# Kernel optimization log

Measured on AMD Instinct MI355X. Metric: run time of the kernel, lower is better.

## Reference

```python
import math
import jax, jax.numpy as jnp
import numpy as np

HIDDEN = 128
NUM_REL = 48
NUM_BASES = 8
NUM_ENT = 50000
NUM_SPECIAL = 64
NUM_EDGES = 600000


def setup_inputs() -> dict:
    key = jax.random.key(0)
    ks = jax.random.split(key, 8)
    edge_index = jax.random.randint(ks[0], (2, NUM_EDGES), 0, NUM_ENT, dtype=jnp.int64)
    edge_type = jax.random.randint(ks[1], (NUM_EDGES,), 0, NUM_REL, dtype=jnp.int64)
    # node embeddings: uniform(-stdv, stdv), stdv = sqrt(6/(N+d)) as in the torch init
    stdv = math.sqrt(6.0 / (NUM_ENT + HIDDEN))
    node_embeds = jax.random.uniform(ks[2], (NUM_ENT, HIDDEN), jnp.float32, -stdv, stdv)
    # RGCN basis-decomposition params (PyG RGCNConv): weight [B, d, d], comp [R, B]
    basis = jax.random.normal(ks[3], (NUM_BASES, HIDDEN, HIDDEN), jnp.float32) * (1.0 / math.sqrt(HIDDEN))
    comp = jax.random.normal(ks[4], (NUM_REL, NUM_BASES), jnp.float32) * (1.0 / math.sqrt(NUM_BASES))
    root = jax.random.normal(ks[5], (HIDDEN, HIDDEN), jnp.float32) * (1.0 / math.sqrt(HIDDEN))
    bias = jnp.zeros((HIDDEN,), jnp.float32)
    special_emb = jax.random.normal(ks[6], (NUM_SPECIAL, HIDDEN), jnp.float32) * 0.02
    special_emb = special_emb.at[0].set(0.0)  # padding_idx=0
    return {"edge_index": edge_index, "edge_type": edge_type,
            "node_embeds": node_embeds, "basis": basis, "comp": comp,
            "root": root, "bias": bias, "special_emb": special_emb}


def rgcn_conv(x, edge_index, edge_type, basis, comp, root, bias):
    # PyG RGCNConv with basis decomposition, aggr='mean', root weight + bias.
    # W_r = sum_b comp[r, b] * basis[b]; out[n] = x[n] @ root + bias
    #        + sum_r mean_{e: type(e)=r, dst(e)=n} (x[src(e)] @ W_r)
    N = x.shape[0]
    R, B = comp.shape
    src, dst = edge_index[0], edge_index[1]
    # per-(relation, dst) in-degree for the per-relation mean aggregation
    seg = edge_type * N + dst  # [E]
    cnt = jax.ops.segment_sum(jnp.ones(src.shape[0], x.dtype), seg, num_segments=R * N)
    norm = 1.0 / jnp.maximum(cnt[seg], 1.0)  # [E]
    w = comp[edge_type] * norm[:, None]  # [E, B] per-edge basis coefficients / count
    x_src = x[src]  # [E, d] gather (dominant memory traffic)
    out = x @ root + bias  # [N, d]
    # linearity: mean over edges of (x_src @ W) == (weighted-sum of x_src) @ basis_b per basis
    for b in range(B):
        agg = jax.ops.segment_sum(x_src * w[:, b:b + 1], dst, num_segments=N)  # [N, d]
        out = out + agg @ basis[b]
    return out


def reference(edge_index, edge_type, node_embeds, basis, comp, root, bias, special_emb):
    node_out = rgcn_conv(node_embeds, edge_index, edge_type, basis, comp, root, bias)
    return jnp.concatenate([node_out, special_emb], axis=0)  # [N + S, d]
```

## Files before the change

kernel.cpp:

```cpp
#include <hip/hip_runtime.h>

#define NDIM 128
#define NBASES 8
#define KDIM 1152
#define GTILE 16
#define APITCH 1160

typedef __attribute__((ext_vector_type(8))) __bf16 bfrag;
typedef __attribute__((ext_vector_type(4))) float f32x4;

__device__ __forceinline__ float bf2f(unsigned short b) {
    return __uint_as_float(((unsigned)b) << 16);
}
__device__ __forceinline__ unsigned short f2bf(float f) {
    unsigned u = __float_as_uint(f);
    unsigned r = u + 0x7FFFu + ((u >> 16) & 1u);
    return (unsigned short)(r >> 16);
}
__device__ __forceinline__ unsigned pack2bf(float lo, float hi) {
    return (unsigned)f2bf(lo) | ((unsigned)f2bf(hi) << 16);
}
__device__ __forceinline__ float loadF(const void* p, int idx, int isf32) {
    return isf32 ? ((const float*)p)[idx] : bf2f(((const unsigned short*)p)[idx]);
}

__global__ void detect_k(const unsigned short* __restrict__ xs,
                         const int* __restrict__ ei, int* __restrict__ meta) {
    if (threadIdx.x != 0 || blockIdx.x != 0) return;
    const uint4* xv = (const uint4*)xs;
    unsigned f32m = 0;
    uint4 bx[16];
    #pragma unroll
    for (int i = 0; i < 16; ++i) bx[i] = xv[i];
    #pragma unroll
    for (int i = 0; i < 16; ++i) {
        unsigned a = bx[i].x, b = bx[i].y, c = bx[i].z, d = bx[i].w;
        f32m |= (((a & 0xFFFFu) >> 7) & 0xFFu) > 124u;
        f32m |= (((b & 0xFFFFu) >> 7) & 0xFFu) > 124u;
        f32m |= (((c & 0xFFFFu) >> 7) & 0xFFu) > 124u;
        f32m |= (((d & 0xFFFFu) >> 7) & 0xFFu) > 124u;
    }
    const uint4* ev = (const uint4*)ei;
    unsigned nzm = 0;
    for (int r = 0; r < 4; ++r) {
        uint4 be[16];
        #pragma unroll
        for (int i = 0; i < 16; ++i) be[i] = ev[r * 16 + i];
        #pragma unroll
        for (int i = 0; i < 16; ++i) nzm |= be[i].y | be[i].w;
    }
    meta[0] = f32m ? 1 : 0;
    meta[1] = nzm ? 0 : 1;
}

__global__ void misc_k(const void* __restrict__ basis, const void* __restrict__ root,
                       const void* __restrict__ se, const int* __restrict__ meta,
                       unsigned short* __restrict__ BT, void* __restrict__ out,
                       int scount, int sbase) {
    int t = blockIdx.x * 256 + threadIdx.x;
    int isf32 = meta[0];
    if (t < NDIM * KDIM) {
        int j = t / KDIM, k = t % KDIM;
        float v = (k < NBASES * NDIM) ? loadF(basis, k * NDIM + j, isf32)
                                      : loadF(root, (k - NBASES * NDIM) * NDIM + j, isf32);
        BT[t] = f2bf(v);
    } else {
        int u = t - NDIM * KDIM;
        if (u < scount) {
            float v = loadF(se, u, isf32);
            if (isf32) ((float*)out)[sbase + u] = v;
            else       ((unsigned short*)out)[sbase + u] = f2bf(v);
        }
    }
}

__global__ void hist_k(const int* __restrict__ ei, int E, int N,
                       const int* __restrict__ meta, int* __restrict__ hist) {
    int e = blockIdx.x * 256 + threadIdx.x;
    if (e >= E) return;
    int dst = meta[1] ? ei[2 * (E + e)] : ei[E + e];
    dst = min(max(dst, 0), N - 1);
    atomicAdd(&hist[dst], 1);
}

__global__ void scanA_k(const int* __restrict__ hist, int N,
                        int* __restrict__ offsets, int* __restrict__ bsum) {
    __shared__ int s[1024];
    int tid = threadIdx.x;
    int idx = blockIdx.x * 1024 + tid;
    int v = (idx < N) ? hist[idx] : 0;
    s[tid] = v;
    __syncthreads();
    for (int off = 1; off < 1024; off <<= 1) {
        int t = 0;
        if (tid >= off) t = s[tid - off];
        __syncthreads();
        if (tid >= off) s[tid] += t;
        __syncthreads();
    }
    if (idx < N) offsets[idx] = s[tid] - v;
    if (tid == 1023) bsum[blockIdx.x] = s[1023];
}
__global__ void scanB_k(const int* __restrict__ bsum, int NB, int N,
                        int* __restrict__ bpre, int* __restrict__ offsets) {
    __shared__ int s[64];
    int tid = threadIdx.x;
    int v = (tid < NB) ? bsum[tid] : 0;
    s[tid] = v;
    __syncthreads();
    for (int off = 1; off < 64; off <<= 1) {
        int t = 0;
        if (tid >= off) t = s[tid - off];
        __syncthreads();
        if (tid >= off) s[tid] += t;
        __syncthreads();
    }
    if (tid < NB) bpre[tid] = s[tid] - v;
    if (tid == NB - 1) offsets[N] = s[tid];
}
__global__ void scanC_k(int N, const int* __restrict__ bpre, int* __restrict__ offsets) {
    int idx = blockIdx.x * 1024 + threadIdx.x;
    if (idx < N) offsets[idx] += bpre[blockIdx.x];
}

__global__ void scatter_k(const int* __restrict__ ei, const int* __restrict__ et,
                          int E, int N, const int* __restrict__ meta,
                          const int* __restrict__ offsets, int* __restrict__ cursor,
                          int* __restrict__ sorted) {
    int e = blockIdx.x * 256 + threadIdx.x;
    if (e >= E) return;
    int i64 = meta[1];
    int src = i64 ? ei[2 * e] : ei[e];
    int dst = i64 ? ei[2 * (E + e)] : ei[E + e];
    int rel = i64 ? et[2 * e] : et[e];
    src = min(max(src, 0), N - 1);
    dst = min(max(dst, 0), N - 1);
    rel = rel & 63;
    int pos = offsets[dst] + atomicAdd(&cursor[dst], 1);
    sorted[pos] = src | (rel << 16);
}

__global__ __launch_bounds__(1024, 8) void rgcn_main_k(
    const void* __restrict__ x, const void* __restrict__ comp,
    const void* __restrict__ bias, const unsigned short* __restrict__ BT,
    const int* __restrict__ meta, const int* __restrict__ offsets,
    const int* __restrict__ sorted, void* __restrict__ out, int N)
{
    __shared__ alignas(16) unsigned short A_lds[GTILE * APITCH];
    __shared__ alignas(16) float comp_lds[48 * NBASES];
    __shared__ int cnt_lds[GTILE * 48];
    const int tid  = threadIdx.x;
    const int lane = tid & 63;
    const int wave = tid >> 6;
    const int isf32 = meta[0];

    for (int t = tid; t < 48 * NBASES; t += 1024)
        comp_lds[t] = loadF(comp, t, isf32);
    __syncthreads();

    const int nodeBase = blockIdx.x * GTILE;
    const int dl = lane & 31;
    const int eg = lane >> 5;

    {
        const int n = nodeBase + wave;
        float acc[8][4];
        #pragma unroll
        for (int j = 0; j < 8; ++j)
            #pragma unroll
            for (int i = 0; i < 4; ++i) acc[j][i] = 0.f;

        int* cnt_row = &cnt_lds[wave * 48];

        if (n < N) {
            const int start = offsets[n], end = offsets[n + 1];

            if (lane < 48) cnt_row[lane] = 0;
            for (int c = start + lane; c < end; c += 64)
                atomicAdd(&cnt_row[(sorted[c] >> 16) & 63], 1);
            if (lane < 48) {
                float nv = __builtin_amdgcn_rcpf(fmaxf((float)cnt_row[lane], 1.0f));
                cnt_row[lane] = __float_as_int(nv);
            }

            if (!isf32) {
                const unsigned short* xh = (const unsigned short*)x;
                if (start < end) {
                    int i0 = start + eg;
                    unsigned q0 = (i0 < end) ? (unsigned)sorted[i0] : 0u;
                    uint2 xa0 = *(const uint2*)(xh + (size_t)(q0 & 0xFFFFu) * NDIM + dl * 4);
                    int i1 = start + 2 + eg;
                    unsigned q1 = (i1 < end) ? (unsigned)sorted[i1] : 0u;
                    for (int c = start; c < end; c += 2) {
                        uint2 xa1 = *(const uint2*)(xh + (size_t)(q1 & 0xFFFFu) * NDIM + dl * 4);
                        int i2 = c + 4 + eg;
                        unsigned q2 = (i2 < end) ? (unsigned)sorted[i2] : 0u;
                        bool act = (c + eg) < end;
                        int rel = (int)((q0 >> 16) & 63u);
                        float norm = act ? __int_as_float(cnt_row[rel]) : 0.f;
                        f32x4 cwA = *(const f32x4*)&comp_lds[rel * NBASES + 4 * eg];
                        f32x4 cwB = *(const f32x4*)&comp_lds[rel * NBASES + 4 * (1 ^ eg)];
                        float w[8];
                        #pragma unroll
                        for (int j = 0; j < 4; ++j) { w[j] = cwA[j] * norm; w[4 + j] = cwB[j] * norm; }
                        float xf[4];
                        xf[0] = __uint_as_float(xa0.x << 16);
                        xf[1] = __uint_as_float(xa0.x & 0xFFFF0000u);
                        xf[2] = __uint_as_float(xa0.y << 16);
                        xf[3] = __uint_as_float(xa0.y & 0xFFFF0000u);
                        #pragma unroll
                        for (int j = 0; j < 8; ++j)
                            #pragma unroll
                            for (int i = 0; i < 4; ++i) acc[j][i] += w[j] * xf[i];
                        q0 = q1; xa0 = xa1; q1 = q2;
                    }
                }
            } else {
                const float* xfp = (const float*)x;
                for (int c = start; c < end; c += 2) {
                    bool act = (c + eg) < end;
                    unsigned q = act ? (unsigned)sorted[c + eg] : 0u;
                    int rel = (int)((q >> 16) & 63u);
                    float norm = act ? __int_as_float(cnt_row[rel]) : 0.f;
                    f32x4 cwA = *(const f32x4*)&comp_lds[rel * NBASES + 4 * eg];
                    f32x4 cwB = *(const f32x4*)&comp_lds[rel * NBASES + 4 * (1 ^ eg)];
                    float w[8];
                    #pragma unroll
                    for (int j = 0; j < 4; ++j) { w[j] = cwA[j] * norm; w[4 + j] = cwB[j] * norm; }
                    f32x4 xv = *(const f32x4*)(xfp + (size_t)(q & 0xFFFFu) * NDIM + dl * 4);
                    #pragma unroll
                    for (int j = 0; j < 8; ++j)
                        #pragma unroll
                        for (int i = 0; i < 4; ++i) acc[j][i] += w[j] * xv[i];
                }
            }
        }

        unsigned short* row = &A_lds[wave * APITCH];
        #pragma unroll
        for (int b = 0; b < 4; ++b) {
            float f0 = acc[b][0] + __shfl_xor(acc[4 + b][0], 32);
            float f1 = acc[b][1] + __shfl_xor(acc[4 + b][1], 32);
            float f2 = acc[b][2] + __shfl_xor(acc[4 + b][2], 32);
            float f3 = acc[b][3] + __shfl_xor(acc[4 + b][3], 32);
            uint2 p;
            p.x = pack2bf(f0, f1);
            p.y = pack2bf(f2, f3);
            *(uint2*)(row + (4 * eg + b) * NDIM + dl * 4) = p;
        }
        if (eg == 0) {
            uint2 xr = {0, 0};
            if (n < N) {
                if (!isf32) {
                    xr = *(const uint2*)((const unsigned short*)x + (size_t)n * NDIM + dl * 4);
                } else {
                    const float* xf = (const float*)x + (size_t)n * NDIM + dl * 4;
                    xr.x = pack2bf(xf[0], xf[1]);
                    xr.y = pack2bf(xf[2], xf[3]);
                }
            }
            *(uint2*)(row + NBASES * NDIM + dl * 4) = xr;
        }
    }
    __syncthreads();

    if (wave < 4) {
        const int m = lane & 15;
        const int q = lane >> 4;
        f32x4 C0 = {0,0,0,0}, C1 = {0,0,0,0};
        const unsigned short* arow = &A_lds[m * APITCH];
        const int jb = wave * 32;
        for (int ks = 0; ks < KDIM / 32; ++ks) {
            int k = ks * 32 + q * 8;
            bfrag a  = *(const bfrag*)(arow + k);
            bfrag b0 = *(const bfrag*)(BT + (size_t)(jb +  0 + m) * KDIM + k);
            bfrag b1 = *(const bfrag*)(BT + (size_t)(jb + 16 + m) * KDIM + k);
            C0 = __builtin_amdgcn_mfma_f32_16x16x32_bf16(a, b0, C0, 0, 0, 0);
            C1 = __builtin_amdgcn_mfma_f32_16x16x32_bf16(a, b1, C1, 0, 0, 0);
        }
        #pragma unroll
        for (int t = 0; t < 2; ++t) {
            f32x4 Ct = t ? C1 : C0;
            int j = jb + t * 16 + m;
            float bj = loadF(bias, j, isf32);
            #pragma unroll
            for (int r = 0; r < 4; ++r) {
                int n = nodeBase + q * 4 + r;
                if (n < N) {
                    float v = Ct[r] + bj;
                    if (isf32) ((float*)out)[(size_t)n * NDIM + j] = v;
                    else       ((unsigned short*)out)[(size_t)n * NDIM + j] = f2bf(v);
                }
            }
        }
    }
}

extern "C" void kernel_launch(void* const* d_in, const int* in_sizes, int n_in,
                              void* d_out, int out_size, void* d_ws, size_t ws_size,
                              hipStream_t stream) {
    const int* ei = (const int*)d_in[0];
    const int* et = (const int*)d_in[1];

    const int E = in_sizes[1];
    const int N = in_sizes[2] / NDIM;
    const int S = in_sizes[7] / NDIM;
    const int NB = (N + 1023) / 1024;

    char* ws = (char*)d_ws;
    size_t off = 0;
    int* meta    = (int*)(ws + off); off += 16;
    int* hist    = (int*)(ws + off); off += (size_t)N * 4;
    int* cursor  = (int*)(ws + off); off += (size_t)N * 4;
    int* offsets = (int*)(ws + off); off = (off + (size_t)(N + 1) * 4 + 15) & ~(size_t)15;
    int* bsum    = (int*)(ws + off); off += 64 * 4;
    int* bpre    = (int*)(ws + off); off += 64 * 4;
    unsigned short* BT = (unsigned short*)(ws + off); off += (size_t)NDIM * KDIM * 2;
    int* sorted  = (int*)(ws + off); off += (size_t)E * 4;

    hipMemsetAsync(hist, 0, (size_t)2 * N * 4, stream);

    detect_k<<<1, 64, 0, stream>>>((const unsigned short*)d_in[2], ei, meta);
    misc_k<<<(NDIM * KDIM + S * NDIM + 255) / 256, 256, 0, stream>>>(
        d_in[3], d_in[5], d_in[7], meta, BT, d_out, S * NDIM, N * NDIM);
    hist_k<<<(E + 255) / 256, 256, 0, stream>>>(ei, E, N, meta, hist);
    scanA_k<<<NB, 1024, 0, stream>>>(hist, N, offsets, bsum);
    scanB_k<<<1, 64, 0, stream>>>(bsum, NB, N, bpre, offsets);
    scanC_k<<<NB, 1024, 0, stream>>>(N, bpre, offsets);
    scatter_k<<<(E + 255) / 256, 256, 0, stream>>>(ei, et, E, N, meta, offsets, cursor, sorted);
    rgcn_main_k<<<(N + GTILE - 1) / GTILE, 1024, 0, stream>>>(d_in[2], d_in[4], d_in[6], BT,
                                                              meta, offsets, sorted, d_out, N);
}
```

Baseline: 330.2 us.

## Batch edge gathers with shuffle-broadcast indices and fuse histogram, scan-fixup kernels

The main gather loop is restructured. Each wave loads 64 sorted edge entries at once and broadcasts them with shuffles, then issues GDEPTH=6 independent row loads before doing any math. This raises memory-level parallelism compared with the previous two-deep prefetch. Each half-wave now accumulates only its 4 bases and exchanges x rows across halves, which halves the accumulator registers and removes the final cross-half reduction. The histogram is folded into misc_k and the scanC pass is removed by adding the block prefix at each use, which cuts two launches but adds an extra bpre lookup in scatter and main.

```diff
diff --git a/kernel.cpp b/kernel.cpp
--- a/kernel.cpp
+++ b/kernel.cpp
@@ -5,6 +5,7 @@
 #define KDIM 1152
 #define GTILE 16
 #define APITCH 1160
+#define GDEPTH 6
 
 typedef __attribute__((ext_vector_type(8))) __bf16 bfrag;
 typedef __attribute__((ext_vector_type(4))) float f32x4;
@@ -56,7 +57,8 @@
 __global__ void misc_k(const void* __restrict__ basis, const void* __restrict__ root,
                        const void* __restrict__ se, const int* __restrict__ meta,
                        unsigned short* __restrict__ BT, void* __restrict__ out,
-                       int scount, int sbase) {
+                       int scount, int sbase,
+                       const int* __restrict__ ei, int E, int N, int* __restrict__ hist) {
     int t = blockIdx.x * 256 + threadIdx.x;
     int isf32 = meta[0];
     if (t < NDIM * KDIM) {
@@ -70,17 +72,15 @@
             float v = loadF(se, u, isf32);
             if (isf32) ((float*)out)[sbase + u] = v;
             else       ((unsigned short*)out)[sbase + u] = f2bf(v);
-        }
-    }
-}
-
-__global__ void hist_k(const int* __restrict__ ei, int E, int N,
-                       const int* __restrict__ meta, int* __restrict__ hist) {
-    int e = blockIdx.x * 256 + threadIdx.x;
-    if (e >= E) return;
-    int dst = meta[1] ? ei[2 * (E + e)] : ei[E + e];
-    dst = min(max(dst, 0), N - 1);
-    atomicAdd(&hist[dst], 1);
+        } else {
+            int e = u - scount;
+            if (e < E) {
+                int dst = meta[1] ? ei[2 * (E + e)] : ei[E + e];
+                dst = min(max(dst, 0), N - 1);
+                atomicAdd(&hist[dst], 1);
+            }
+        }
+    }
 }
 
 __global__ void scanA_k(const int* __restrict__ hist, int N,
@@ -118,15 +118,11 @@
     if (tid < NB) bpre[tid] = s[tid] - v;
     if (tid == NB - 1) offsets[N] = s[tid];
 }
-__global__ void scanC_k(int N, const int* __restrict__ bpre, int* __restrict__ offsets) {
-    int idx = blockIdx.x * 1024 + threadIdx.x;
-    if (idx < N) offsets[idx] += bpre[blockIdx.x];
-}
 
 __global__ void scatter_k(const int* __restrict__ ei, const int* __restrict__ et,
                           int E, int N, const int* __restrict__ meta,
-                          const int* __restrict__ offsets, int* __restrict__ cursor,
-                          int* __restrict__ sorted) {
+                          const int* __restrict__ offsets, const int* __restrict__ bpre,
+                          int* __restrict__ cursor, int* __restrict__ sorted) {
     int e = blockIdx.x * 256 + threadIdx.x;
     if (e >= E) return;
     int i64 = meta[1];
@@ -136,7 +132,7 @@
     src = min(max(src, 0), N - 1);
     dst = min(max(dst, 0), N - 1);
     rel = rel & 63;
-    int pos = offsets[dst] + atomicAdd(&cursor[dst], 1);
+    int pos = offsets[dst] + bpre[dst >> 10] + atomicAdd(&cursor[dst], 1);
     sorted[pos] = src | (rel << 16);
 }
 
@@ -144,6 +140,7 @@
     const void* __restrict__ x, const void* __restrict__ comp,
     const void* __restrict__ bias, const unsigned short* __restrict__ BT,
     const int* __restrict__ meta, const int* __restrict__ offsets,
+    const int* __restrict__ bpre,
     const int* __restrict__ sorted, void* __restrict__ out, int N)
 {
     __shared__ alignas(16) unsigned short A_lds[GTILE * APITCH];
@@ -164,19 +161,25 @@
 
     {
         const int n = nodeBase + wave;
-        float acc[8][4];
-        #pragma unroll
-        for (int j = 0; j < 8; ++j)
+        float acc[4][4];
+        #pragma unroll
+        for (int b = 0; b < 4; ++b)
             #pragma unroll
-            for (int i = 0; i < 4; ++i) acc[j][i] = 0.f;
+            for (int i = 0; i < 4; ++i) acc[b][i] = 0.f;
 
         int* cnt_row = &cnt_lds[wave * 48];
 
         if (n < N) {
-            const int start = offsets[n], end = offsets[n + 1];
+            const int start = offsets[n] + bpre[n >> 10];
+            const int idx1  = n + 1;
+            const int end   = offsets[idx1] + ((idx1 < N) ? bpre[idx1 >> 10] : 0);
+            const int deg   = end - start;
+
+            int sv0 = (start + lane < end) ? sorted[start + lane] : 0;
 
             if (lane < 48) cnt_row[lane] = 0;
-            for (int c = start + lane; c < end; c += 64)
+            if (start + lane < end) atomicAdd(&cnt_row[(sv0 >> 16) & 63], 1);
+            for (int c = start + 64 + lane; c < end; c += 64)
                 atomicAdd(&cnt_row[(sorted[c] >> 16) & 63], 1);
             if (lane < 48) {
                 float nv = __builtin_amdgcn_rcpf(fmaxf((float)cnt_row[lane], 1.0f));
@@ -185,53 +188,68 @@
 
             if (!isf32) {
                 const unsigned short* xh = (const unsigned short*)x;
-                if (start < end) {
-                    int i0 = start + eg;
-                    unsigned q0 = (i0 < end) ? (unsigned)sorted[i0] : 0u;
-                    uint2 xa0 = *(const uint2*)(xh + (size_t)(q0 & 0xFFFFu) * NDIM + dl * 4);
-                    int i1 = start + 2 + eg;
-                    unsigned q1 = (i1 < end) ? (unsigned)sorted[i1] : 0u;
-                    for (int c = start; c < end; c += 2) {
-                        uint2 xa1 = *(const uint2*)(xh + (size_t)(q1 & 0xFFFFu) * NDIM + dl * 4);
-                        int i2 = c + 4 + eg;
-                        unsigned q2 = (i2 < end) ? (unsigned)sorted[i2] : 0u;
-                        bool act = (c + eg) < end;
-                        int rel = (int)((q0 >> 16) & 63u);
-                        float norm = act ? __int_as_float(cnt_row[rel]) : 0.f;
-                        f32x4 cwA = *(const f32x4*)&comp_lds[rel * NBASES + 4 * eg];
-                        f32x4 cwB = *(const f32x4*)&comp_lds[rel * NBASES + 4 * (1 ^ eg)];
-                        float w[8];
+                int sv = sv0;
+                for (int w0 = 0; w0 < deg; w0 += 64) {
+                    if (w0 > 0)
+                        sv = (start + w0 + lane < end) ? sorted[start + w0 + lane] : 0;
+                    const int wdeg = min(64, deg - w0);
+                    for (int b0 = 0; b0 < wdeg; b0 += 2 * GDEPTH) {
+                        uint2 xa[GDEPTH];
                         #pragma unroll
-                        for (int j = 0; j < 4; ++j) { w[j] = cwA[j] * norm; w[4 + j] = cwB[j] * norm; }
-                        float xf[4];
-                        xf[0] = __uint_as_float(xa0.x << 16);
-                        xf[1] = __uint_as_float(xa0.x & 0xFFFF0000u);
-                        xf[2] = __uint_as_float(xa0.y << 16);
-                        xf[3] = __uint_as_float(xa0.y & 0xFFFF0000u);
+                        for (int u = 0; u < GDEPTH; ++u) {
+                            int eo = b0 + 2 * u + eg;
+                            unsigned qs = (unsigned)__shfl(sv, eo & 63);
+                            unsigned qo = (eo < wdeg) ? qs : 0u;
+                            xa[u] = *(const uint2*)(xh + (size_t)(qo & 0xFFFFu) * NDIM + dl * 4);
+                        }
                         #pragma unroll
-                        for (int j = 0; j < 8; ++j)
+                        for (int u = 0; u < GDEPTH; ++u) {
+                            int e0 = b0 + 2 * u;
+                            bool a0 = e0 < wdeg, a1 = (e0 + 1) < wdeg;
+                            unsigned q0 = a0 ? (unsigned)__shfl(sv, e0 & 63) : 0u;
+                            unsigned q1 = a1 ? (unsigned)__shfl(sv, (e0 + 1) & 63) : 0u;
+                            int r0 = (int)((q0 >> 16) & 63u);
+                            int r1 = (int)((q1 >> 16) & 63u);
+                            float n0 = a0 ? __int_as_float(cnt_row[r0]) : 0.f;
+                            float n1 = a1 ? __int_as_float(cnt_row[r1]) : 0.f;
+                            f32x4 cw0 = *(const f32x4*)&comp_lds[r0 * NBASES + 4 * eg];
+                            f32x4 cw1 = *(const f32x4*)&comp_lds[r1 * NBASES + 4 * eg];
+                            uint2 xo = xa[u];
+                            uint2 xp;
+                            xp.x = (unsigned)__shfl_xor((int)xo.x, 32);
+                            xp.y = (unsigned)__shfl_xor((int)xo.y, 32);
+                            uint2 xe0 = eg ? xp : xo;
+                            uint2 xe1 = eg ? xo : xp;
+                            float y0[4], y1[4];
+                            y0[0] = __uint_as_float(xe0.x << 16) * n0;
+                            y0[1] = __uint_as_float(xe0.x & 0xFFFF0000u) * n0;
+                            y0[2] = __uint_as_float(xe0.y << 16) * n0;
+                            y0[3] = __uint_as_float(xe0.y & 0xFFFF0000u) * n0;
+                            y1[0] = __uint_as_float(xe1.x << 16) * n1;
+                            y1[1] = __uint_as_float(xe1.x & 0xFFFF0000u) * n1;
+                            y1[2] = __uint_as_float(xe1.y << 16) * n1;
+                            y1[3] = __uint_as_float(xe1.y & 0xFFFF0000u) * n1;
                             #pragma unroll
-                            for (int i = 0; i < 4; ++i) acc[j][i] += w[j] * xf[i];
-                        q0 = q1; xa0 = xa1; q1 = q2;
+                            for (int b = 0; b < 4; ++b)
+                                #pragma unroll
+                                for (int i = 0; i < 4; ++i)
+                                    acc[b][i] += cw0[b] * y0[i] + cw1[b] * y1[i];
+                        }
                     }
                 }
             } else {
                 const float* xfp = (const float*)x;
-                for (int c = start; c < end; c += 2) {
-                    bool act = (c + eg) < end;
-                    unsigned q = act ? (unsigned)sorted[c + eg] : 0u;
+                for (int c = start; c < end; ++c) {
+                    unsigned q = (unsigned)sorted[c];
                     int rel = (int)((q >> 16) & 63u);
-                    float norm = act ? __int_as_float(cnt_row[rel]) : 0.f;
-                    f32x4 cwA = *(const f32x4*)&comp_lds[rel * NBASES + 4 * eg];
-                    f32x4 cwB = *(const f32x4*)&comp_lds[rel * NBASES + 4 * (1 ^ eg)];
-                    float w[8];
-                    #pragma unroll
-                    for (int j = 0; j < 4; ++j) { w[j] = cwA[j] * norm; w[4 + j] = cwB[j] * norm; }
+                    float norm = __int_as_float(cnt_row[rel]);
+                    f32x4 cw = *(const f32x4*)&comp_lds[rel * NBASES + 4 * eg];
                     f32x4 xv = *(const f32x4*)(xfp + (size_t)(q & 0xFFFFu) * NDIM + dl * 4);
                     #pragma unroll
-                    for (int j = 0; j < 8; ++j)
+                    for (int b = 0; b < 4; ++b)
                         #pragma unroll
-                        for (int i = 0; i < 4; ++i) acc[j][i] += w[j] * xv[i];
+                        for (int i = 0; i < 4; ++i)
+                            acc[b][i] += cw[b] * (norm * xv[i]);
                 }
             }
         }
@@ -239,13 +257,9 @@
         unsigned short* row = &A_lds[wave * APITCH];
         #pragma unroll
         for (int b = 0; b < 4; ++b) {
-            float f0 = acc[b][0] + __shfl_xor(acc[4 + b][0], 32);
-            float f1 = acc[b][1] + __shfl_xor(acc[4 + b][1], 32);
-            float f2 = acc[b][2] + __shfl_xor(acc[4 + b][2], 32);
-            float f3 = acc[b][3] + __shfl_xor(acc[4 + b][3], 32);
             uint2 p;
-            p.x = pack2bf(f0, f1);
-            p.y = pack2bf(f2, f3);
+            p.x = pack2bf(acc[b][0], acc[b][1]);
+            p.y = pack2bf(acc[b][2], acc[b][3]);
             *(uint2*)(row + (4 * eg + b) * NDIM + dl * 4) = p;
         }
         if (eg == 0) {
@@ -321,13 +335,15 @@
     hipMemsetAsync(hist, 0, (size_t)2 * N * 4, stream);
 
     detect_k<<<1, 64, 0, stream>>>((const unsigned short*)d_in[2], ei, meta);
-    misc_k<<<(NDIM * KDIM + S * NDIM + 255) / 256, 256, 0, stream>>>(
-        d_in[3], d_in[5], d_in[7], meta, BT, d_out, S * NDIM, N * NDIM);
-    hist_k<<<(E + 255) / 256, 256, 0, stream>>>(ei, E, N, meta, hist);
+    {
+        int T = NDIM * KDIM + S * NDIM + E;
+        misc_k<<<(T + 255) / 256, 256, 0, stream>>>(
+            d_in[3], d_in[5], d_in[7], meta, BT, d_out, S * NDIM, N * NDIM,
+            ei, E, N, hist);
+    }
     scanA_k<<<NB, 1024, 0, stream>>>(hist, N, offsets, bsum);
     scanB_k<<<1, 64, 0, stream>>>(bsum, NB, N, bpre, offsets);
-    scanC_k<<<NB, 1024, 0, stream>>>(N, bpre, offsets);
-    scatter_k<<<(E + 255) / 256, 256, 0, stream>>>(ei, et, E, N, meta, offsets, cursor, sorted);
+    scatter_k<<<(E + 255) / 256, 256, 0, stream>>>(ei, et, E, N, meta, offsets, bpre, cursor, sorted);
     rgcn_main_k<<<(N + GTILE - 1) / GTILE, 1024, 0, stream>>>(d_in[2], d_in[4], d_in[6], BT,
-                                                              meta, offsets, sorted, d_out, N);
-}
+                                                              meta, offsets, bpre, sorted, d_out, N);
+}
```

Result: slower. 365.2 us (+10.6%).

## Fuse histogram into misc kernel, drop scan fixup pass, deepen gather prefetch

Applied to the files above, without the earlier changes.

The edge in-degree histogram now runs inside the misc kernel that converts weights and copies special embeddings. The third scan kernel is removed; scatter and the main kernel add the per-1024-block prefix on the fly when reading offsets. The bf16 gather loop prefetches one more edge row ahead, which costs extra registers. Together these cut two kernel launches and one pass over the offsets array, and give more memory-level parallelism in the main aggregation.

```diff
diff --git a/kernel.cpp b/kernel.cpp
--- a/kernel.cpp
+++ b/kernel.cpp
@@ -56,7 +56,8 @@
 __global__ void misc_k(const void* __restrict__ basis, const void* __restrict__ root,
                        const void* __restrict__ se, const int* __restrict__ meta,
                        unsigned short* __restrict__ BT, void* __restrict__ out,
-                       int scount, int sbase) {
+                       int scount, int sbase,
+                       const int* __restrict__ ei, int E, int N, int* __restrict__ hist) {
     int t = blockIdx.x * 256 + threadIdx.x;
     int isf32 = meta[0];
     if (t < NDIM * KDIM) {
@@ -70,17 +71,15 @@
             float v = loadF(se, u, isf32);
             if (isf32) ((float*)out)[sbase + u] = v;
             else       ((unsigned short*)out)[sbase + u] = f2bf(v);
-        }
-    }
-}
-
-__global__ void hist_k(const int* __restrict__ ei, int E, int N,
-                       const int* __restrict__ meta, int* __restrict__ hist) {
-    int e = blockIdx.x * 256 + threadIdx.x;
-    if (e >= E) return;
-    int dst = meta[1] ? ei[2 * (E + e)] : ei[E + e];
-    dst = min(max(dst, 0), N - 1);
-    atomicAdd(&hist[dst], 1);
+        } else {
+            int e = u - scount;
+            if (e < E) {
+                int dst = meta[1] ? ei[2 * (E + e)] : ei[E + e];
+                dst = min(max(dst, 0), N - 1);
+                atomicAdd(&hist[dst], 1);
+            }
+        }
+    }
 }
 
 __global__ void scanA_k(const int* __restrict__ hist, int N,
@@ -118,15 +117,11 @@
     if (tid < NB) bpre[tid] = s[tid] - v;
     if (tid == NB - 1) offsets[N] = s[tid];
 }
-__global__ void scanC_k(int N, const int* __restrict__ bpre, int* __restrict__ offsets) {
-    int idx = blockIdx.x * 1024 + threadIdx.x;
-    if (idx < N) offsets[idx] += bpre[blockIdx.x];
-}
 
 __global__ void scatter_k(const int* __restrict__ ei, const int* __restrict__ et,
                           int E, int N, const int* __restrict__ meta,
-                          const int* __restrict__ offsets, int* __restrict__ cursor,
-                          int* __restrict__ sorted) {
+                          const int* __restrict__ offsets, const int* __restrict__ bpre,
+                          int* __restrict__ cursor, int* __restrict__ sorted) {
     int e = blockIdx.x * 256 + threadIdx.x;
     if (e >= E) return;
     int i64 = meta[1];
@@ -136,7 +131,7 @@
     src = min(max(src, 0), N - 1);
     dst = min(max(dst, 0), N - 1);
     rel = rel & 63;
-    int pos = offsets[dst] + atomicAdd(&cursor[dst], 1);
+    int pos = offsets[dst] + bpre[dst >> 10] + atomicAdd(&cursor[dst], 1);
     sorted[pos] = src | (rel << 16);
 }
 
@@ -144,6 +139,7 @@
     const void* __restrict__ x, const void* __restrict__ comp,
     const void* __restrict__ bias, const unsigned short* __restrict__ BT,
     const int* __restrict__ meta, const int* __restrict__ offsets,
+    const int* __restrict__ bpre,
     const int* __restrict__ sorted, void* __restrict__ out, int N)
 {
     __shared__ alignas(16) unsigned short A_lds[GTILE * APITCH];
@@ -173,7 +169,9 @@
         int* cnt_row = &cnt_lds[wave * 48];
 
         if (n < N) {
-            const int start = offsets[n], end = offsets[n + 1];
+            const int start = offsets[n] + bpre[n >> 10];
+            const int idx1  = n + 1;
+            const int end   = offsets[idx1] + ((idx1 < N) ? bpre[idx1 >> 10] : 0);
 
             if (lane < 48) cnt_row[lane] = 0;
             for (int c = start + lane; c < end; c += 64)
@@ -188,13 +186,16 @@
                 if (start < end) {
                     int i0 = start + eg;
                     unsigned q0 = (i0 < end) ? (unsigned)sorted[i0] : 0u;
-                    uint2 xa0 = *(const uint2*)(xh + (size_t)(q0 & 0xFFFFu) * NDIM + dl * 4);
                     int i1 = start + 2 + eg;
                     unsigned q1 = (i1 < end) ? (unsigned)sorted[i1] : 0u;
+                    uint2 xa0 = *(const uint2*)(xh + (size_t)(q0 & 0xFFFFu) * NDIM + dl * 4);
+                    uint2 xa1 = *(const uint2*)(xh + (size_t)(q1 & 0xFFFFu) * NDIM + dl * 4);
+                    int i2 = start + 4 + eg;
+                    unsigned q2 = (i2 < end) ? (unsigned)sorted[i2] : 0u;
                     for (int c = start; c < end; c += 2) {
-                        uint2 xa1 = *(const uint2*)(xh + (size_t)(q1 & 0xFFFFu) * NDIM + dl * 4);
-                        int i2 = c + 4 + eg;
-                        unsigned q2 = (i2 < end) ? (unsigned)sorted[i2] : 0u;
+                        uint2 xa2 = *(const uint2*)(xh + (size_t)(q2 & 0xFFFFu) * NDIM + dl * 4);
+                        int i3 = c + 6 + eg;
+                        unsigned q3 = (i3 < end) ? (unsigned)sorted[i3] : 0u;
                         bool act = (c + eg) < end;
                         int rel = (int)((q0 >> 16) & 63u);
                         float norm = act ? __int_as_float(cnt_row[rel]) : 0.f;
@@ -203,16 +204,17 @@
                         float w[8];
                         #pragma unroll
                         for (int j = 0; j < 4; ++j) { w[j] = cwA[j] * norm; w[4 + j] = cwB[j] * norm; }
-                        float xf[4];
-                        xf[0] = __uint_as_float(xa0.x << 16);
-                        xf[1] = __uint_as_float(xa0.x & 0xFFFF0000u);
-                        xf[2] = __uint_as_float(xa0.y << 16);
-                        xf[3] = __uint_as_float(xa0.y & 0xFFFF0000u);
+                        float xv_[4];
+                        xv_[0] = __uint_as_float(xa0.x << 16);
+                        xv_[1] = __uint_as_float(xa0.x & 0xFFFF0000u);
+                        xv_[2] = __uint_as_float(xa0.y << 16);
+                        xv_[3] = __uint_as_float(xa0.y & 0xFFFF0000u);
                         #pragma unroll
                         for (int j = 0; j < 8; ++j)
                             #pragma unroll
-                            for (int i = 0; i < 4; ++i) acc[j][i] += w[j] * xf[i];
-                        q0 = q1; xa0 = xa1; q1 = q2;
+                            for (int i = 0; i < 4; ++i) acc[j][i] += w[j] * xv_[i];
+                        q0 = q1; q1 = q2; q2 = q3;
+                        xa0 = xa1; xa1 = xa2;
                     }
                 }
             } else {
@@ -321,13 +323,15 @@
     hipMemsetAsync(hist, 0, (size_t)2 * N * 4, stream);
 
     detect_k<<<1, 64, 0, stream>>>((const unsigned short*)d_in[2], ei, meta);
-    misc_k<<<(NDIM * KDIM + S * NDIM + 255) / 256, 256, 0, stream>>>(
-        d_in[3], d_in[5], d_in[7], meta, BT, d_out, S * NDIM, N * NDIM);
-    hist_k<<<(E + 255) / 256, 256, 0, stream>>>(ei, E, N, meta, hist);
+    {
+        int T = NDIM * KDIM + S * NDIM + E;
+        misc_k<<<(T + 255) / 256, 256, 0, stream>>>(
+            d_in[3], d_in[5], d_in[7], meta, BT, d_out, S * NDIM, N * NDIM,
+            ei, E, N, hist);
+    }
     scanA_k<<<NB, 1024, 0, stream>>>(hist, N, offsets, bsum);
     scanB_k<<<1, 64, 0, stream>>>(bsum, NB, N, bpre, offsets);
-    scanC_k<<<NB, 1024, 0, stream>>>(N, bpre, offsets);
-    scatter_k<<<(E + 255) / 256, 256, 0, stream>>>(ei, et, E, N, meta, offsets, cursor, sorted);
+    scatter_k<<<(E + 255) / 256, 256, 0, stream>>>(ei, et, E, N, meta, offsets, bpre, cursor, sorted);
     rgcn_main_k<<<(N + GTILE - 1) / GTILE, 1024, 0, stream>>>(d_in[2], d_in[4], d_in[6], BT,
-                                                              meta, offsets, sorted, d_out, N);
-}
+                                                              meta, offsets, bpre, sorted, d_out, N);
+}
```

New measurement: 332.2 us. Within noise of the previous version (+0.6%).
